# Kernel optimization log

Hardware: AMD Instinct MI355X
Metric: run time of the kernel (lower is better)

The kernel has to match this reference:

```python
import jax, jax.numpy as jnp
import numpy as np

B, S, D, H = 16, 2048, 1024, 16
CLIP = 8
NC = S // CLIP  # num_clips = 256


def setup_inputs() -> dict:
    key = jax.random.key(0)
    ks = jax.random.split(key, 24)

    def w(k, shape):
        return jax.random.normal(k, shape, dtype=jnp.float32) * 0.02

    inp = {
        "x": jax.random.normal(ks[0], (B, S, D), dtype=jnp.float32),
        "mask": jnp.ones((B, 1, S), dtype=jnp.int32),
    }
    names = ["sa_q", "sa_k", "sa_v", "sa_o", "ta_q", "ta_k", "ta_v", "ta_o"]
    for i, n in enumerate(names):
        inp[n + "_w"] = w(ks[2 * i + 1], (D, D))
        inp[n + "_b"] = w(ks[2 * i + 2], (D,))
    inp["fuse_w"] = w(ks[17], (2 * D, D))
    inp["fuse_b"] = w(ks[18], (D,))
    return inp


def _mha(x, m, wq, bq, wk, bk, wv, bv, wo, bo):
    # x: [..., L, D]; m: broadcastable to [..., 1, L, L] (or [..., 1, 1, L])
    lead = x.shape[:-2]
    L, d = x.shape[-2], x.shape[-1]
    dk = d // H

    def proj(wt, bt):
        y = x @ wt + bt                      # [..., L, D]
        y = y.reshape(*lead, L, H, dk)
        return jnp.moveaxis(y, -2, -3)       # [..., H, L, dk]

    q, k, v = proj(wq, bq), proj(wk, bk), proj(wv, bv)
    scores = jnp.einsum('...hqd,...hkd->...hqk', q, k) / np.sqrt(dk)
    scores = jnp.where(m == 0, -jnp.inf, scores)
    att = jax.nn.softmax(scores, axis=-1)
    out = jnp.einsum('...hqk,...hkd->...hqd', att, v)
    out = jnp.moveaxis(out, -3, -2).reshape(*lead, L, d)
    return out @ wo + bo


def reference(x, mask,
              sa_q_w, sa_q_b, sa_k_w, sa_k_b, sa_v_w, sa_v_b, sa_o_w, sa_o_b,
              ta_q_w, ta_q_b, ta_k_w, ta_k_b, ta_v_w, ta_v_b, ta_o_w, ta_o_b,
              fuse_w, fuse_b):
    # x: [B, S, D], mask: [B, 1, S]; S divisible by CLIP so no padding branch
    x4 = x.reshape(B, NC, CLIP, D)
    m = mask.reshape(B, NC, CLIP)

    # spatial: attend within each clip (batched over num_clips)
    # mask per clip [B,1,clip_len] -> unsqueeze head dim -> [B,nc,1,1,clip_len]
    m_s = m[:, :, None, None, :]
    spatial = _mha(x4, m_s, sa_q_w, sa_q_b, sa_k_w, sa_k_b,
                   sa_v_w, sa_v_b, sa_o_w, sa_o_b)        # [B, NC, CLIP, D]

    # temporal: attend across clips at each within-clip position j
    xt = jnp.swapaxes(x4, 1, 2)                            # [B, CLIP, NC, D]
    m_t = jnp.swapaxes(m, 1, 2)[:, :, None, None, :]       # [B, CLIP, 1, 1, NC]
    temporal = _mha(xt, m_t, ta_q_w, ta_q_b, ta_k_w, ta_k_b,
                    ta_v_w, ta_v_b, ta_o_w, ta_o_b)        # [B, CLIP, NC, D]
    temporal = jnp.swapaxes(temporal, 1, 2)                # [B, NC, CLIP, D]

    combined = jnp.concatenate([spatial, temporal], axis=-1)  # [B, NC, CLIP, 2D]
    fused = combined @ fuse_w + fuse_b                        # [B, NC, CLIP, D]
    return fused.reshape(B, NC * CLIP, D)
```

## Files before the change

kernel.cpp:

```cpp
#include <hip/hip_runtime.h>


typedef __bf16 bf16x8 __attribute__((ext_vector_type(8)));
typedef float f32x4 __attribute__((ext_vector_type(4)));

typedef const unsigned int __attribute__((address_space(1)))* gas_p;
typedef unsigned int __attribute__((address_space(3)))* las_p;

__device__ __forceinline__ void gld_lds16(const void* g, void* l) {
  __builtin_amdgcn_global_load_lds((gas_p)g, (las_p)l, 16, 0, 0);
}

__global__ void detect_dtype(const unsigned short* __restrict__ x,
                             int* __restrict__ flag) {
  __shared__ int acc;
  if (threadIdx.x == 0) acc = 0;
  __syncthreads();
  int big = 0;
  for (int i = threadIdx.x; i < 8192; i += 256) {
    const int ex = (x[2 * i] >> 7) & 0xFF;
    big += (ex >= 0xC0);
  }
  atomicAdd(&acc, big);
  __syncthreads();
  if (threadIdx.x == 0) flag[0] = (acc > 128) ? 1 : 0;
}

__global__ __launch_bounds__(256) void cvt_bf16(const void* __restrict__ src,
                                                __bf16* __restrict__ dst, long n,
                                                const int* __restrict__ flag) {
  const long i = ((long)blockIdx.x * 256 + threadIdx.x) * 8;
  if (i >= n) return;
  if (*flag) {
    const f32x4* s = (const f32x4*)((const float*)src + i);
    const f32x4 a = s[0], b = s[1];
    bf16x8 v;
    v[0] = (__bf16)a[0]; v[1] = (__bf16)a[1]; v[2] = (__bf16)a[2]; v[3] = (__bf16)a[3];
    v[4] = (__bf16)b[0]; v[5] = (__bf16)b[1]; v[6] = (__bf16)b[2]; v[7] = (__bf16)b[3];
    *(bf16x8*)(dst + i) = v;
  } else {
    *(bf16x8*)(dst + i) = *(const bf16x8*)((const __bf16*)src + i);
  }
}

__device__ __forceinline__ float load_f(const void* p, long i, int f) {
  return f ? ((const float*)p)[i] : (float)(((const __bf16*)p)[i]);
}

__global__ __launch_bounds__(256) void gemm_bt(
    const __bf16* __restrict__ A, int lda,
    const __bf16* __restrict__ Bt, int ldb,
    const float* __restrict__ bias,
    void* __restrict__ Cv, long elemOff, int ldc, int K,
    const int* __restrict__ ofl) {
  __shared__ __attribute__((aligned(16))) __bf16 sA[2][4096];
  __shared__ __attribute__((aligned(16))) __bf16 sB[2][4096];
  const int t = threadIdx.x;
  const int lane = t & 63;
  const int wave = t >> 6;
  const int wm = wave >> 1, wn = wave & 1;
  const int quad = lane >> 4, l16 = lane & 15;

  int bx = blockIdx.x, by = blockIdx.y;
  const int gx = gridDim.x, gy = gridDim.y;
  if ((gx & 7) == 0) {
    const int d = blockIdx.x + gx * blockIdx.y;
    const int c = d & 7, s = d >> 3;
    by = s % gy;
    bx = c * (gx >> 3) + s / gy;
  }
  const long mBase = (long)bx * 128;
  const long nBase = (long)by * 128;

  f32x4 acc[4][4] = {};

  const int arow = t >> 2;
  const int acol = (t & 3) * 8;
  const __bf16* gA0 = A + (mBase + arow) * (long)lda + acol;
  const __bf16* gA1 = gA0 + 64 * (long)lda;
  const __bf16* gB0 = Bt + (nBase + arow) * (long)ldb + acol;
  const __bf16* gB1 = gB0 + 64 * (long)ldb;

  const int fAoff = (wm * 64 + l16) * 32 + quad * 8;
  const int fBoff = (wn * 64 + l16) * 32 + quad * 8;

  gld_lds16(gA0, &sA[0][t * 8]);
  gld_lds16(gA1, &sA[0][2048 + t * 8]);
  gld_lds16(gB0, &sB[0][t * 8]);
  gld_lds16(gB1, &sB[0][2048 + t * 8]);
  __syncthreads();

  int cur = 0;
  for (int k0 = 0; k0 < K; k0 += 32) {
    if (k0 + 32 < K) {
      const int nxt = cur ^ 1;
      gld_lds16(gA0 + k0 + 32, &sA[nxt][t * 8]);
      gld_lds16(gA1 + k0 + 32, &sA[nxt][2048 + t * 8]);
      gld_lds16(gB0 + k0 + 32, &sB[nxt][t * 8]);
      gld_lds16(gB1 + k0 + 32, &sB[nxt][2048 + t * 8]);
    }
    bf16x8 af[4], bfr[4];
#pragma unroll
    for (int i = 0; i < 4; ++i) af[i] = *(const bf16x8*)(&sA[cur][fAoff + i * 512]);
#pragma unroll
    for (int j = 0; j < 4; ++j) bfr[j] = *(const bf16x8*)(&sB[cur][fBoff + j * 512]);
#pragma unroll
    for (int i = 0; i < 4; ++i)
#pragma unroll
      for (int j = 0; j < 4; ++j)
        acc[i][j] = __builtin_amdgcn_mfma_f32_16x16x32_bf16(af[i], bfr[j],
                                                            acc[i][j], 0, 0, 0);
    __syncthreads();
    cur ^= 1;
  }

  const int f32out = (ofl != nullptr) && (*ofl != 0);
  __bf16* Cb = (__bf16*)Cv + elemOff;
  float* Cf = (float*)Cv + elemOff;
#pragma unroll
  for (int i = 0; i < 4; ++i) {
    const long gr0 = mBase + wm * 64 + i * 16 + quad * 4;
#pragma unroll
    for (int j = 0; j < 4; ++j) {
      const long gc = nBase + wn * 64 + j * 16 + l16;
      const float bv = bias ? bias[gc] : 0.f;
#pragma unroll
      for (int r = 0; r < 4; ++r) {
        const float val = acc[i][j][r] + bv;
        const long idx = (gr0 + r) * (long)ldc + gc;
        if (f32out) Cf[idx] = val;
        else Cb[idx] = (__bf16)val;
      }
    }
  }
}

__global__ void transpose_k(const __bf16* __restrict__ in,
                            __bf16* __restrict__ out, int R, int C) {
  __shared__ __bf16 tile[32][33];
  const int c0 = blockIdx.x * 32, r0 = blockIdx.y * 32;
  const int tx = threadIdx.x & 31, ty = threadIdx.x >> 5;
  for (int rr = ty; rr < 32; rr += 8)
    tile[rr][tx] = in[(long)(r0 + rr) * C + c0 + tx];
  __syncthreads();
  for (int rr = ty; rr < 32; rr += 8)
    out[(long)(c0 + rr) * R + r0 + tx] = tile[tx][rr];
}

__global__ void bias_cvt6(const void* b0, const void* b1, const void* b2,
                          const void* b3, const void* b4, const void* b5,
                          float* out, const int* __restrict__ flag) {
  const void* ps[6] = {b0, b1, b2, b3, b4, b5};
  const int which = blockIdx.y;
  const int i = blockIdx.x * 256 + threadIdx.x;
  out[which * 1024 + i] = load_f(ps[which], i, *flag);
}

__global__ __launch_bounds__(256) void bias_fuse(
    const __bf16* __restrict__ fuse_t, const void* __restrict__ fb,
    const void* __restrict__ sob, const void* __restrict__ tob,
    float* __restrict__ out, const int* __restrict__ flag) {
  const int wave = threadIdx.x >> 6, lane = threadIdx.x & 63;
  const int n = blockIdx.x * 4 + wave;
  const int f = *flag;
  const __bf16* row = fuse_t + (long)n * 2048;
  float s = 0.f;
#pragma unroll
  for (int base = 0; base < 2048; base += 512) {
    const int k = base + lane * 8;
    const bf16x8 rv = *(const bf16x8*)(row + k);
#pragma unroll
    for (int e = 0; e < 8; ++e) {
      const int kk = k + e;
      const float w = (base < 1024) ? load_f(sob, kk, f)
                                    : load_f(tob, kk - 1024, f);
      s += w * (float)rv[e];
    }
  }
#pragma unroll
  for (int off = 1; off < 64; off <<= 1) s += __shfl_xor(s, off);
  if (lane == 0) out[n] = s + load_f(fb, n, f);
}

__global__ __launch_bounds__(256) void attn_spatial(
    const __bf16* __restrict__ Q, const __bf16* __restrict__ K,
    const __bf16* __restrict__ V, __bf16* __restrict__ A2) {
  __shared__ __attribute__((aligned(16))) __bf16 sQ[4][512], sK[4][512], sV[4][512];
  __shared__ float sP[4][64];
  const int wave = threadIdx.x >> 6, lane = threadIdx.x & 63;
  const int unit = blockIdx.x * 4 + wave;
  const int h = unit & 15;
  const int c = (unit >> 4) & 255;
  const int b = unit >> 12;
  const long rowbase = ((long)b * 256 + c) * 8;
  const int colbase = h * 64;
  const int i = lane >> 3, j = lane & 7;
  const int lc = j * 8;
  const long goff = (rowbase + i) * 1024 + colbase + lc;
  *(bf16x8*)&sQ[wave][i * 64 + lc] = *(const bf16x8*)(Q + goff);
  *(bf16x8*)&sK[wave][i * 64 + lc] = *(const bf16x8*)(K + goff);
  *(bf16x8*)&sV[wave][i * 64 + lc] = *(const bf16x8*)(V + goff);
  __syncthreads();
  float s = 0.f;
#pragma unroll
  for (int d8 = 0; d8 < 8; ++d8) {
    bf16x8 qv = *(const bf16x8*)&sQ[wave][i * 64 + d8 * 8];
    bf16x8 kv = *(const bf16x8*)&sK[wave][j * 64 + d8 * 8];
#pragma unroll
    for (int e = 0; e < 8; ++e) s += (float)qv[e] * (float)kv[e];
  }
  s *= 0.125f;
  float mx = s;
  mx = fmaxf(mx, __shfl_xor(mx, 1));
  mx = fmaxf(mx, __shfl_xor(mx, 2));
  mx = fmaxf(mx, __shfl_xor(mx, 4));
  float pe = __expf(s - mx);
  float sum = pe;
  sum += __shfl_xor(sum, 1);
  sum += __shfl_xor(sum, 2);
  sum += __shfl_xor(sum, 4);
  sP[wave][i * 8 + j] = pe / sum;
  __syncthreads();
  float o[8] = {};
#pragma unroll
  for (int jj = 0; jj < 8; ++jj) {
    float pj = sP[wave][i * 8 + jj];
    bf16x8 vv = *(const bf16x8*)&sV[wave][jj * 64 + lc];
#pragma unroll
    for (int e = 0; e < 8; ++e) o[e] += pj * (float)vv[e];
  }
  bf16x8 ov;
#pragma unroll
  for (int e = 0; e < 8; ++e) ov[e] = (__bf16)o[e];
  *(bf16x8*)(A2 + (rowbase + i) * 2048 + colbase + lc) = ov;
}

__global__ __launch_bounds__(256, 2) void attn_temporal(
    const __bf16* __restrict__ Q, const __bf16* __restrict__ K,
    const __bf16* __restrict__ V, __bf16* __restrict__ A2) {
  __shared__ __attribute__((aligned(16))) __bf16 sK[64 * 72];
  __shared__ __attribute__((aligned(16))) __bf16 sVt[64 * 72];
  __shared__ __attribute__((aligned(16))) __bf16 sP[4][64 * 72];

  const int unit = blockIdx.x;
  const int h = unit & 15;
  const int t8 = (unit >> 4) & 7;
  const int b = unit >> 7;
  const long Base = (long)b * 2048 + t8;
  const int colbase = h * 64;

  const int t = threadIdx.x;
  const int wave = t >> 6;
  const int lane = t & 63;
  const int quad = lane >> 4;
  const int l16 = lane & 15;
  __bf16* sPw = sP[wave];

  bf16x8 qf[4][2];
#pragma unroll
  for (int i = 0; i < 4; ++i) {
    const long qrow = Base + (long)(wave * 64 + i * 16 + l16) * 8;
#pragma unroll
    for (int kc = 0; kc < 2; ++kc)
      qf[i][kc] = *(const bf16x8*)(Q + qrow * 1024 + colbase + kc * 32 + quad * 8);
  }

  f32x4 o[4][4] = {};
  f32x4 m[4], l[4];
#pragma unroll
  for (int i = 0; i < 4; ++i)
#pragma unroll
    for (int e = 0; e < 4; ++e) { m[i][e] = -1e30f; l[i][e] = 0.f; }

  const int kk = t >> 2;
  const int dg = (t & 3) * 16;

  for (int kb = 0; kb < 4; ++kb) {
    __syncthreads();
    const long krow = Base + (long)(kb * 64 + kk) * 8;
    const __bf16* kg = K + krow * 1024 + colbase + dg;
    const __bf16* vg = V + krow * 1024 + colbase + dg;
    const bf16x8 k0 = *(const bf16x8*)(kg);
    const bf16x8 k1 = *(const bf16x8*)(kg + 8);
    const bf16x8 v0 = *(const bf16x8*)(vg);
    const bf16x8 v1 = *(const bf16x8*)(vg + 8);
    *(bf16x8*)&sK[kk * 72 + dg] = k0;
    *(bf16x8*)&sK[kk * 72 + dg + 8] = k1;
#pragma unroll
    for (int e = 0; e < 8; ++e) sVt[(dg + e) * 72 + kk] = v0[e];
#pragma unroll
    for (int e = 0; e < 8; ++e) sVt[(dg + 8 + e) * 72 + kk] = v1[e];
    __syncthreads();

    bf16x8 kf[4][2];
#pragma unroll
    for (int j = 0; j < 4; ++j)
#pragma unroll
      for (int kc = 0; kc < 2; ++kc)
        kf[j][kc] = *(const bf16x8*)&sK[(j * 16 + l16) * 72 + kc * 32 + quad * 8];

#pragma unroll
    for (int i = 0; i < 4; ++i) {
      f32x4 sv[4];
#pragma unroll
      for (int j = 0; j < 4; ++j) {
        f32x4 z = {};
        sv[j] = __builtin_amdgcn_mfma_f32_16x16x32_bf16(qf[i][0], kf[j][0], z, 0, 0, 0);
        sv[j] = __builtin_amdgcn_mfma_f32_16x16x32_bf16(qf[i][1], kf[j][1], sv[j], 0, 0, 0);
        sv[j] *= 0.125f;
      }
      f32x4 bm = sv[0];
#pragma unroll
      for (int j = 1; j < 4; ++j)
#pragma unroll
        for (int e = 0; e < 4; ++e) bm[e] = fmaxf(bm[e], sv[j][e]);
#pragma unroll
      for (int off = 1; off < 16; off <<= 1)
#pragma unroll
        for (int e = 0; e < 4; ++e) bm[e] = fmaxf(bm[e], __shfl_xor(bm[e], off));
      f32x4 mn, fct;
#pragma unroll
      for (int e = 0; e < 4; ++e) {
        mn[e] = fmaxf(m[i][e], bm[e]);
        fct[e] = __expf(m[i][e] - mn[e]);
      }
      m[i] = mn;
      l[i] *= fct;
#pragma unroll
      for (int jd = 0; jd < 4; ++jd) o[i][jd] *= fct;
      f32x4 rs = {};
#pragma unroll
      for (int j = 0; j < 4; ++j) {
        f32x4 p;
#pragma unroll
        for (int e = 0; e < 4; ++e) p[e] = __expf(sv[j][e] - mn[e]);
        rs += p;
#pragma unroll
        for (int r = 0; r < 4; ++r)
          sPw[(i * 16 + quad * 4 + r) * 72 + j * 16 + l16] = (__bf16)p[r];
      }
#pragma unroll
      for (int off = 1; off < 16; off <<= 1)
#pragma unroll
        for (int e = 0; e < 4; ++e) rs[e] += __shfl_xor(rs[e], off);
      l[i] += rs;
    }

    asm volatile("s_waitcnt lgkmcnt(0)" ::: "memory");

    bf16x8 vf[4][2];
#pragma unroll
    for (int jd = 0; jd < 4; ++jd)
#pragma unroll
      for (int kc = 0; kc < 2; ++kc)
        vf[jd][kc] = *(const bf16x8*)&sVt[(jd * 16 + l16) * 72 + kc * 32 + quad * 8];
#pragma unroll
    for (int i = 0; i < 4; ++i) {
      const bf16x8 pf0 = *(const bf16x8*)&sPw[(i * 16 + l16) * 72 + quad * 8];
      const bf16x8 pf1 = *(const bf16x8*)&sPw[(i * 16 + l16) * 72 + 32 + quad * 8];
#pragma unroll
      for (int jd = 0; jd < 4; ++jd) {
        o[i][jd] = __builtin_amdgcn_mfma_f32_16x16x32_bf16(pf0, vf[jd][0], o[i][jd], 0, 0, 0);
        o[i][jd] = __builtin_amdgcn_mfma_f32_16x16x32_bf16(pf1, vf[jd][1], o[i][jd], 0, 0, 0);
      }
    }
  }

#pragma unroll
  for (int i = 0; i < 4; ++i) {
    f32x4 inv;
#pragma unroll
    for (int e = 0; e < 4; ++e) inv[e] = 1.f / l[i][e];
#pragma unroll
    for (int jd = 0; jd < 4; ++jd) {
#pragma unroll
      for (int r = 0; r < 4; ++r) {
        const long q = wave * 64 + i * 16 + quad * 4 + r;
        A2[(Base + q * 8) * 2048 + 1024 + colbase + jd * 16 + l16] =
            (__bf16)(o[i][jd][r] * inv[r]);
      }
    }
  }
}

extern "C" void kernel_launch(void* const* d_in, const int* in_sizes, int n_in,
                              void* d_out, int out_size, void* d_ws, size_t ws_size,
                              hipStream_t stream) {
  (void)in_sizes; (void)n_in; (void)out_size;
  const void* x    = d_in[0];
  const void* w_sq = d_in[2];
  const void* b_sq = d_in[3];
  const void* w_sk = d_in[4];
  const void* b_sk = d_in[5];
  const void* w_sv = d_in[6];
  const void* b_sv = d_in[7];
  const void* w_so = d_in[8];
  const void* b_so = d_in[9];
  const void* w_tq = d_in[10];
  const void* b_tq = d_in[11];
  const void* w_tk = d_in[12];
  const void* b_tk = d_in[13];
  const void* w_tv = d_in[14];
  const void* b_tv = d_in[15];
  const void* w_to = d_in[16];
  const void* b_to = d_in[17];
  const void* w_f  = d_in[18];
  const void* b_f  = d_in[19];

  char* p = (char*)d_ws;
  auto alloc = [&](size_t nbytes) {
    char* r = p;
    p += (nbytes + 255) & ~(size_t)255;
    return r;
  };
  int*    flag   = (int*)alloc(256);
  __bf16* xb     = (__bf16*)alloc((size_t)16 * 2048 * 1024 * 2);
  __bf16* wt[6];
  for (int i = 0; i < 6; ++i) wt[i] = (__bf16*)alloc((size_t)1024 * 1024 * 2);
  __bf16* wso_c  = (__bf16*)alloc((size_t)1024 * 1024 * 2);
  __bf16* wto_c  = (__bf16*)alloc((size_t)1024 * 1024 * 2);
  __bf16* fuse_t = (__bf16*)alloc((size_t)1024 * 2048 * 2);
  __bf16* mct    = (__bf16*)alloc((size_t)1024 * 2048 * 2);
  float*  biasf  = (float*)alloc((size_t)7 * 1024 * 4);
  __bf16* tmp    = (__bf16*)alloc((size_t)2048 * 1024 * 2);

  const size_t used = (size_t)(p - (char*)d_ws);
  const size_t per_b = (size_t)2048 * (3 * 1024 * 2 + 2048 * 2);
  int nb = 16;
  while (nb > 1 && used + (size_t)nb * per_b + 4096 > ws_size) nb >>= 1;

  __bf16* Qb = (__bf16*)alloc((size_t)nb * 2048 * 1024 * 2);
  __bf16* Kb = (__bf16*)alloc((size_t)nb * 2048 * 1024 * 2);
  __bf16* Vb = (__bf16*)alloc((size_t)nb * 2048 * 1024 * 2);
  __bf16* A2 = (__bf16*)alloc((size_t)nb * 2048 * 2048 * 2);

  const long NX = (long)16 * 2048 * 1024;
  const long NW = (long)1024 * 1024;
  const long NF = (long)2048 * 1024;

  detect_dtype<<<dim3(1), 256, 0, stream>>>((const unsigned short*)x, flag);
  cvt_bf16<<<dim3(NX / 2048), 256, 0, stream>>>(x, xb, NX, flag);
  const void* wraw[6] = {w_sq, w_sk, w_sv, w_tq, w_tk, w_tv};
  for (int i = 0; i < 6; ++i) {
    cvt_bf16<<<dim3(NW / 2048), 256, 0, stream>>>(wraw[i], tmp, NW, flag);
    transpose_k<<<dim3(32, 32), 256, 0, stream>>>(tmp, wt[i], 1024, 1024);
  }
  cvt_bf16<<<dim3(NW / 2048), 256, 0, stream>>>(w_so, wso_c, NW, flag);
  cvt_bf16<<<dim3(NW / 2048), 256, 0, stream>>>(w_to, wto_c, NW, flag);
  cvt_bf16<<<dim3(NF / 2048), 256, 0, stream>>>(w_f, tmp, NF, flag);
  transpose_k<<<dim3(32, 64), 256, 0, stream>>>(tmp, fuse_t, 2048, 1024);
  bias_cvt6<<<dim3(4, 6), 256, 0, stream>>>(b_sq, b_sk, b_sv, b_tq, b_tk, b_tv,
                                            biasf, flag);
  gemm_bt<<<dim3(8, 8), 256, 0, stream>>>(fuse_t, 2048, wso_c, 1024, nullptr,
                                          mct, 0, 2048, 1024, nullptr);
  gemm_bt<<<dim3(8, 8), 256, 0, stream>>>(fuse_t + 1024, 2048, wto_c, 1024, nullptr,
                                          mct, 1024, 2048, 1024, nullptr);
  bias_fuse<<<dim3(256), 256, 0, stream>>>(fuse_t, b_f, b_so, b_to,
                                           biasf + 6 * 1024, flag);

  for (int cb = 0; cb < 16; cb += nb) {
    const __bf16* xa = xb + (size_t)cb * 2048 * 1024;
    const int M = nb * 2048;
    const dim3 gg(M / 128, 8);
    gemm_bt<<<gg, 256, 0, stream>>>(xa, 1024, wt[0], 1024, biasf + 0,    Qb, 0, 1024, 1024, nullptr);
    gemm_bt<<<gg, 256, 0, stream>>>(xa, 1024, wt[1], 1024, biasf + 1024, Kb, 0, 1024, 1024, nullptr);
    gemm_bt<<<gg, 256, 0, stream>>>(xa, 1024, wt[2], 1024, biasf + 2048, Vb, 0, 1024, 1024, nullptr);
    attn_spatial<<<dim3(nb * 1024), 256, 0, stream>>>(Qb, Kb, Vb, A2);
    gemm_bt<<<gg, 256, 0, stream>>>(xa, 1024, wt[3], 1024, biasf + 3072, Qb, 0, 1024, 1024, nullptr);
    gemm_bt<<<gg, 256, 0, stream>>>(xa, 1024, wt[4], 1024, biasf + 4096, Kb, 0, 1024, 1024, nullptr);
    gemm_bt<<<gg, 256, 0, stream>>>(xa, 1024, wt[5], 1024, biasf + 5120, Vb, 0, 1024, 1024, nullptr);
    attn_temporal<<<dim3(nb * 128), 256, 0, stream>>>(Qb, Kb, Vb, A2);
    gemm_bt<<<gg, 256, 0, stream>>>(A2, 2048, mct, 2048, biasf + 6144,
                                    d_out, (long)cb * 2048 * 1024, 1024, 2048, flag);
  }
}
```

Before: 1.339 ms.

## Add 256x256-tile pipelined GEMM kernel for projection and fuse GEMMs

Introduces gemm256, a 512-thread kernel that computes 256x256 output tiles with swizzled LDS, direct global-to-LDS loads staged in quarter pieces interleaved with MFMA phases, setprio hints, and block-index remapping for cache locality. All per-chunk projection and fuse GEMMs switch from the 128x128 gemm_bt to this kernel. The larger tile is meant to raise arithmetic intensity and overlap loads with compute, at the cost of 64K-element LDS use, higher register pressure and fewer blocks in the grid.

```diff
diff --git a/kernel.cpp b/kernel.cpp
--- a/kernel.cpp
+++ b/kernel.cpp
@@ -10,6 +10,14 @@
 __device__ __forceinline__ void gld_lds16(const void* g, void* l) {
   __builtin_amdgcn_global_load_lds((gas_p)g, (las_p)l, 16, 0, 0);
 }
+
+#define FENCE() asm volatile("" ::: "memory")
+#define BARRIER()                  \
+  do {                             \
+    FENCE();                       \
+    __builtin_amdgcn_s_barrier();  \
+    FENCE();                       \
+  } while (0)
 
 __global__ void detect_dtype(const unsigned short* __restrict__ x,
                              int* __restrict__ flag) {
@@ -120,6 +128,158 @@
 #pragma unroll
   for (int i = 0; i < 4; ++i) {
     const long gr0 = mBase + wm * 64 + i * 16 + quad * 4;
+#pragma unroll
+    for (int j = 0; j < 4; ++j) {
+      const long gc = nBase + wn * 64 + j * 16 + l16;
+      const float bv = bias ? bias[gc] : 0.f;
+#pragma unroll
+      for (int r = 0; r < 4; ++r) {
+        const float val = acc[i][j][r] + bv;
+        const long idx = (gr0 + r) * (long)ldc + gc;
+        if (f32out) Cf[idx] = val;
+        else Cb[idx] = (__bf16)val;
+      }
+    }
+  }
+}
+
+__device__ __forceinline__ void stage_piece(
+    const __bf16* __restrict__ A, long lda, const __bf16* __restrict__ Bt,
+    long ldb, long mBase, long nBase, __bf16* lds, int t, int p, int T,
+    int NT) {
+  if (T >= NT) T = NT - 1;
+  const int srow = t >> 3;
+  const int scol = ((t & 7) ^ ((t >> 3) & 7)) * 8;
+  const long col = (long)T * 64 + scol;
+  const int h = p & 1;
+  __bf16* lbase = lds + (p < 2 ? 0 : 32768) + (T & 1) * 16384 + h * 8192 + t * 8;
+#pragma unroll
+  for (int L = 0; L < 2; ++L) {
+    const int grow = h * 128 + L * 64 + srow;
+    const __bf16* g = (p < 2) ? (A + (mBase + grow) * lda + col)
+                              : (Bt + (nBase + grow) * ldb + col);
+    gld_lds16(g, lbase + L * 4096);
+  }
+}
+
+__global__ __launch_bounds__(512, 2) void gemm256(
+    const __bf16* __restrict__ A, int lda_i,
+    const __bf16* __restrict__ Bt, int ldb_i,
+    const float* __restrict__ bias,
+    void* __restrict__ Cv, long elemOff, int ldc, int K,
+    const int* __restrict__ ofl) {
+  __shared__ __attribute__((aligned(16))) __bf16 lds[65536];
+  const long lda = lda_i, ldb = ldb_i;
+  const int t = threadIdx.x;
+  const int wave = t >> 6, lane = t & 63;
+  const int quad = lane >> 4, l16 = lane & 15;
+  const int wm = wave >> 2, wn = wave & 3;
+
+  int bx = blockIdx.x, by = blockIdx.y;
+  const int gx = gridDim.x, gy = gridDim.y;
+  if ((gx & 7) == 0) {
+    const int d = blockIdx.x + gx * blockIdx.y;
+    const int c = d & 7, s = d >> 3;
+    by = s % gy;
+    bx = c * (gx >> 3) + s / gy;
+  }
+  const long mBase = (long)bx * 256;
+  const long nBase = (long)by * 256;
+  const int NT = K >> 6;
+
+  f32x4 acc[8][4] = {};
+
+  const int aB = wm * 8192 + l16 * 64;
+  const int bB = 32768 + (wn >> 1) * 8192 + ((wn & 1) * 64 + l16) * 64;
+  const int swz0 = (quad ^ (l16 & 7)) * 8;
+  const int swz1 = ((4 + quad) ^ (l16 & 7)) * 8;
+
+  stage_piece(A, lda, Bt, ldb, mBase, nBase, lds, t, 0, 0, NT);
+  stage_piece(A, lda, Bt, ldb, mBase, nBase, lds, t, 1, 0, NT);
+  stage_piece(A, lda, Bt, ldb, mBase, nBase, lds, t, 2, 0, NT);
+  stage_piece(A, lda, Bt, ldb, mBase, nBase, lds, t, 3, 0, NT);
+  stage_piece(A, lda, Bt, ldb, mBase, nBase, lds, t, 0, 1, NT);
+  stage_piece(A, lda, Bt, ldb, mBase, nBase, lds, t, 1, 1, NT);
+  asm volatile("s_waitcnt vmcnt(4)" ::: "memory");
+  BARRIER();
+
+  for (int kt = 0; kt < NT; ++kt) {
+    const int bo = (kt & 1) * 16384;
+    const __bf16* aL = lds + bo + aB;
+    const __bf16* bL = lds + bo + bB;
+    bf16x8 af[4][2], bf[4][2], ag[4][2];
+
+#pragma unroll
+    for (int i = 0; i < 4; ++i) {
+      af[i][0] = *(const bf16x8*)(aL + i * 1024 + swz0);
+      af[i][1] = *(const bf16x8*)(aL + i * 1024 + swz1);
+    }
+#pragma unroll
+    for (int j = 0; j < 4; ++j) {
+      bf[j][0] = *(const bf16x8*)(bL + j * 1024 + swz0);
+      bf[j][1] = *(const bf16x8*)(bL + j * 1024 + swz1);
+    }
+    stage_piece(A, lda, Bt, ldb, mBase, nBase, lds, t, 2, kt + 1, NT);
+    BARRIER();
+    __builtin_amdgcn_s_setprio(1);
+#pragma unroll
+    for (int i = 0; i < 4; ++i)
+#pragma unroll
+      for (int j = 0; j < 4; ++j)
+        acc[i][j] = __builtin_amdgcn_mfma_f32_16x16x32_bf16(af[i][0], bf[j][0],
+                                                            acc[i][j], 0, 0, 0);
+    __builtin_amdgcn_s_setprio(0);
+    BARRIER();
+
+    stage_piece(A, lda, Bt, ldb, mBase, nBase, lds, t, 3, kt + 1, NT);
+    BARRIER();
+    __builtin_amdgcn_s_setprio(1);
+#pragma unroll
+    for (int i = 0; i < 4; ++i)
+#pragma unroll
+      for (int j = 0; j < 4; ++j)
+        acc[i][j] = __builtin_amdgcn_mfma_f32_16x16x32_bf16(af[i][1], bf[j][1],
+                                                            acc[i][j], 0, 0, 0);
+    __builtin_amdgcn_s_setprio(0);
+    BARRIER();
+
+#pragma unroll
+    for (int i = 0; i < 4; ++i) {
+      ag[i][0] = *(const bf16x8*)(aL + (i + 4) * 1024 + swz0);
+      ag[i][1] = *(const bf16x8*)(aL + (i + 4) * 1024 + swz1);
+    }
+    BARRIER();
+    __builtin_amdgcn_s_setprio(1);
+#pragma unroll
+    for (int i = 0; i < 4; ++i)
+#pragma unroll
+      for (int j = 0; j < 4; ++j)
+        acc[i + 4][j] = __builtin_amdgcn_mfma_f32_16x16x32_bf16(
+            ag[i][0], bf[j][0], acc[i + 4][j], 0, 0, 0);
+    __builtin_amdgcn_s_setprio(0);
+    BARRIER();
+
+    stage_piece(A, lda, Bt, ldb, mBase, nBase, lds, t, 0, kt + 2, NT);
+    stage_piece(A, lda, Bt, ldb, mBase, nBase, lds, t, 1, kt + 2, NT);
+    BARRIER();
+    __builtin_amdgcn_s_setprio(1);
+#pragma unroll
+    for (int i = 0; i < 4; ++i)
+#pragma unroll
+      for (int j = 0; j < 4; ++j)
+        acc[i + 4][j] = __builtin_amdgcn_mfma_f32_16x16x32_bf16(
+            ag[i][1], bf[j][1], acc[i + 4][j], 0, 0, 0);
+    __builtin_amdgcn_s_setprio(0);
+    asm volatile("s_waitcnt vmcnt(4)" ::: "memory");
+    BARRIER();
+  }
+
+  const int f32out = (ofl != nullptr) && (*ofl != 0);
+  __bf16* Cb = (__bf16*)Cv + elemOff;
+  float* Cf = (float*)Cv + elemOff;
+#pragma unroll
+  for (int i = 0; i < 8; ++i) {
+    const long gr0 = mBase + wm * 128 + i * 16 + quad * 4;
 #pragma unroll
     for (int j = 0; j < 4; ++j) {
       const long gc = nBase + wn * 64 + j * 16 + l16;
@@ -461,16 +621,16 @@
   for (int cb = 0; cb < 16; cb += nb) {
     const __bf16* xa = xb + (size_t)cb * 2048 * 1024;
     const int M = nb * 2048;
-    const dim3 gg(M / 128, 8);
-    gemm_bt<<<gg, 256, 0, stream>>>(xa, 1024, wt[0], 1024, biasf + 0,    Qb, 0, 1024, 1024, nullptr);
-    gemm_bt<<<gg, 256, 0, stream>>>(xa, 1024, wt[1], 1024, biasf + 1024, Kb, 0, 1024, 1024, nullptr);
-    gemm_bt<<<gg, 256, 0, stream>>>(xa, 1024, wt[2], 1024, biasf + 2048, Vb, 0, 1024, 1024, nullptr);
+    const dim3 gg(M / 256, 4);
+    gemm256<<<gg, 512, 0, stream>>>(xa, 1024, wt[0], 1024, biasf + 0,    Qb, 0, 1024, 1024, nullptr);
+    gemm256<<<gg, 512, 0, stream>>>(xa, 1024, wt[1], 1024, biasf + 1024, Kb, 0, 1024, 1024, nullptr);
+    gemm256<<<gg, 512, 0, stream>>>(xa, 1024, wt[2], 1024, biasf + 2048, Vb, 0, 1024, 1024, nullptr);
     attn_spatial<<<dim3(nb * 1024), 256, 0, stream>>>(Qb, Kb, Vb, A2);
-    gemm_bt<<<gg, 256, 0, stream>>>(xa, 1024, wt[3], 1024, biasf + 3072, Qb, 0, 1024, 1024, nullptr);
-    gemm_bt<<<gg, 256, 0, stream>>>(xa, 1024, wt[4], 1024, biasf + 4096, Kb, 0, 1024, 1024, nullptr);
-    gemm_bt<<<gg, 256, 0, stream>>>(xa, 1024, wt[5], 1024, biasf + 5120, Vb, 0, 1024, 1024, nullptr);
+    gemm256<<<gg, 512, 0, stream>>>(xa, 1024, wt[3], 1024, biasf + 3072, Qb, 0, 1024, 1024, nullptr);
+    gemm256<<<gg, 512, 0, stream>>>(xa, 1024, wt[4], 1024, biasf + 4096, Kb, 0, 1024, 1024, nullptr);
+    gemm256<<<gg, 512, 0, stream>>>(xa, 1024, wt[5], 1024, biasf + 5120, Vb, 0, 1024, 1024, nullptr);
     attn_temporal<<<dim3(nb * 128), 256, 0, stream>>>(Qb, Kb, Vb, A2);
-    gemm_bt<<<gg, 256, 0, stream>>>(A2, 2048, mct, 2048, biasf + 6144,
+    gemm256<<<gg, 512, 0, stream>>>(A2, 2048, mct, 2048, biasf + 6144,
                                     d_out, (long)cb * 2048 * 1024, 1024, 2048, flag);
   }
 }
```

New measurement: 1.164 ms. -13.1%, faster.
